# Kernel tuning notes

Hardware: AMD Instinct MI355X
Metric: run time of the kernel (lower is better)

Reference implementation:

```python
import jax, jax.numpy as jnp
import numpy as np

B, T, C = 1, 2048, 1024
H, HKV, DH, WIN = 16, 4, 64, 128
EPS = 1e-5


def rotate_half(x):
    x1, x2 = jnp.split(x, 2, axis=-1)
    return jnp.concatenate((-x2, x1), axis=-1)


def setup_inputs() -> dict:
    key = jax.random.key(0)
    ks = jax.random.split(key, 8)
    s = 0.02
    return {
        "x": jax.random.normal(ks[0], (B, T, C), dtype=jnp.float32),
        "Wq": jax.random.normal(ks[1], (C, H * DH), dtype=jnp.float32) * s,
        "Wk": jax.random.normal(ks[2], (C, HKV * DH), dtype=jnp.float32) * s,
        "Wv": jax.random.normal(ks[3], (C, HKV * DH), dtype=jnp.float32) * s,
        "Wc": jax.random.normal(ks[4], (C, C), dtype=jnp.float32) * s,
        "Wg": jax.random.normal(ks[5], (C, H), dtype=jnp.float32) * s,
        "bg": jax.random.normal(ks[6], (H,), dtype=jnp.float32) * s,
        "rms_w": jnp.ones((C,), dtype=jnp.float32),
    }


def reference(x, Wq, Wk, Wv, Wc, Wg, bg, rms_w):
    n_rep = H // HKV
    # projections -> [B, heads, T, DH]
    q = (x @ Wq).reshape(B, T, H, DH).transpose(0, 2, 1, 3)
    k = (x @ Wk).reshape(B, T, HKV, DH).transpose(0, 2, 1, 3)
    v = (x @ Wv).reshape(B, T, HKV, DH).transpose(0, 2, 1, 3)
    # rotary embedding (freqs duplicated across the two halves)
    inv_freq = 1.0 / (10000.0 ** (jnp.arange(0, DH, 2, dtype=jnp.float32) / DH))
    freqs = jnp.arange(T, dtype=jnp.float32)[:, None] * inv_freq[None, :]
    emb = jnp.concatenate((freqs, freqs), axis=-1)  # [T, DH]
    cos, sin = jnp.cos(emb)[None, None], jnp.sin(emb)[None, None]
    q = q * cos + rotate_half(q) * sin
    k = k * cos + rotate_half(k) * sin
    # GQA: repeat kv heads (contiguous repeat matches torch expand+reshape)
    k = jnp.repeat(k, n_rep, axis=1)
    v = jnp.repeat(v, n_rep, axis=1)
    # gated decay
    gate_logits = (x @ Wg + bg).reshape(B, T, H, 1).transpose(0, 2, 1, 3)  # [B,H,T,1]
    log_alpha = jax.nn.log_sigmoid(gate_logits)
    log_in_scale = jax.nn.log_sigmoid(-gate_logits)
    k_scaled = k * jnp.exp(log_in_scale)
    la_cum = jnp.cumsum(log_alpha, axis=2)                  # [B,H,T,1]
    log_decay = la_cum - jnp.swapaxes(la_cum, 2, 3)         # [B,H,T,T]
    causal = jnp.triu(jnp.ones((T, T), dtype=bool), k=1)
    decay = jnp.exp(jnp.where(causal, -jnp.inf, log_decay))
    scores = jnp.einsum('bhtd,bhsd->bhts', q, k_scaled)
    y_global = jnp.einsum('bhts,bhsd->bhtd', scores * decay, v)
    nb = T // WIN
    qb = q.reshape(B, H, nb, WIN, DH)
    kb = k.reshape(B, H, nb, WIN, DH)
    vb = v.reshape(B, H, nb, WIN, DH)
    att = jnp.einsum('bhnqd,bhnkd->bhnqk', qb, kb) / jnp.sqrt(jnp.float32(DH))
    wmask = jnp.triu(jnp.ones((WIN, WIN), dtype=bool), k=1)
    att = jax.nn.softmax(jnp.where(wmask, -jnp.inf, att), axis=-1)
    y_local = jnp.einsum('bhnqk,bhnkd->bhnqd', att, vb).reshape(B, H, T, DH)
    # fuse, RMSNorm, output projection
    y = (y_global + y_local).transpose(0, 2, 1, 3).reshape(B, T, C)
    y = y * jax.lax.rsqrt(jnp.mean(y * y, axis=-1, keepdims=True) + EPS) * rms_w
    return y @ Wc
```

## Files before the change

### kernel.cpp

```cpp
#include <hip/hip_runtime.h>
#include <hip/hip_bf16.h>


typedef __attribute__((ext_vector_type(8))) short bf16x8;
typedef __attribute__((ext_vector_type(4))) float f32x4;

#define MFMA16(a, b, c) __builtin_amdgcn_mfma_f32_16x16x32_bf16(a, b, c, 0, 0, 0)
#define LN10000_OVER_32 0.28782313662425575f

__device__ __forceinline__ short f2b(float f) {
  __hip_bfloat16 h = __float2bfloat16(f);
  return *reinterpret_cast<short*>(&h);
}
__device__ __forceinline__ float b2f(short s) {
  return __uint_as_float(((unsigned)(unsigned short)s) << 16);
}
__device__ __forceinline__ void gload16(const void* g, void* l) {
  __builtin_amdgcn_global_load_lds(
      (const __attribute__((address_space(1))) void*)g,
      (__attribute__((address_space(3))) void*)l, 16, 0, 0);
}

__device__ __forceinline__ void transpose_cvt_body(
    const float* __restrict__ src, short* __restrict__ dst, int R, int C,
    int bx, int by, float* ts ) {
  int c0 = bx * 32, r0 = by * 32;
  int tr = threadIdx.x >> 3, tc = (threadIdx.x & 7) * 4;
  float4 v = *(const float4*)&src[(size_t)(r0 + tr) * C + c0 + tc];
  ts[tr * 33 + tc] = v.x;
  ts[tr * 33 + tc + 1] = v.y;
  ts[tr * 33 + tc + 2] = v.z;
  ts[tr * 33 + tc + 3] = v.w;
  __syncthreads();
  alignas(8) short o[4];
#pragma unroll
  for (int i = 0; i < 4; ++i) o[i] = f2b(ts[(tc + i) * 33 + tr]);
  *(uint2*)&dst[(size_t)(c0 + tr) * R + r0 + tc] = *(uint2*)o;
}

__global__ __launch_bounds__(256) void prep_fused(
    const float* __restrict__ x, const float* __restrict__ Wq,
    const float* __restrict__ Wk, const float* __restrict__ Wv,
    const float* __restrict__ Wc, const float* __restrict__ Wg,
    const float* __restrict__ bg, short* __restrict__ xb,
    short* __restrict__ wqkvT, short* __restrict__ wcT,
    float* __restrict__ g) {
  __shared__ float ts[32 * 33];
  const int j = blockIdx.x;
  const int tid = threadIdx.x;
  if (j < 2048) {
    const int t = j;
    const int h = tid & 15, chunk = tid >> 4;
    const float* xr = x + (size_t)t * 1024 + chunk * 64;
    const float* wg = Wg + (size_t)chunk * 64 * 16 + h;
    float acc = 0.f;
#pragma unroll
    for (int c = 0; c < 64; c += 4) {
      float4 xv = *(const float4*)(xr + c);
      acc = fmaf(xv.x, wg[(c + 0) * 16], acc);
      acc = fmaf(xv.y, wg[(c + 1) * 16], acc);
      acc = fmaf(xv.z, wg[(c + 2) * 16], acc);
      acc = fmaf(xv.w, wg[(c + 3) * 16], acc);
    }
    ts[chunk * 16 + h] = acc;
    __syncthreads();
    if (tid < 16) {
      float s = bg[tid];
#pragma unroll
      for (int i = 0; i < 16; ++i) s += ts[i * 16 + tid];
      g[t * 16 + tid] = s;
    }
  } else if (j < 3072) {
    int i = ((j - 2048) * 256 + tid) * 8;
    float4 a = *(const float4*)(x + i);
    float4 b = *(const float4*)(x + i + 4);
    alignas(16) short o[8] = {f2b(a.x), f2b(a.y), f2b(a.z), f2b(a.w),
                              f2b(b.x), f2b(b.y), f2b(b.z), f2b(b.w)};
    *(float4*)(xb + i) = *(float4*)o;
  } else if (j < 4096) {
    int jj = j - 3072;
    transpose_cvt_body(Wq, wqkvT, 1024, 1024, jj & 31, jj >> 5, ts);
  } else if (j < 4352) {
    int jj = j - 4096;
    transpose_cvt_body(Wk, wqkvT + 1024 * 1024, 1024, 256, jj & 7, jj >> 3, ts);
  } else if (j < 4608) {
    int jj = j - 4352;
    transpose_cvt_body(Wv, wqkvT + 1280 * 1024, 1024, 256, jj & 7, jj >> 3, ts);
  } else {
    int jj = j - 4608;
    transpose_cvt_body(Wc, wcT, 1024, 1024, jj & 31, jj >> 5, ts);
  }
}

__global__ __launch_bounds__(256) void qkv_gemm_fused(
    const short* __restrict__ A, const short* __restrict__ Bt,
    short* __restrict__ qkvb, short* __restrict__ vtb,
    const float* __restrict__ g, float* __restrict__ lac,
    float* __restrict__ insc) {
  __shared__ short As[64 * 64];
  __shared__ short Bs[64 * 64];
  __shared__ float part[256];
  const int id = blockIdx.x;
  const int tid = threadIdx.x;
  if (id >= 768) {
    const int h = id - 768;
    float vals[8];
    float local = 0.f;
#pragma unroll
    for (int i = 0; i < 8; ++i) {
      int t = tid * 8 + i;
      float gv = g[t * 16 + h];
      float la = (gv > 0.f) ? -log1pf(expf(-gv)) : (gv - log1pf(expf(gv)));
      insc[h * 2048 + t] = 1.f / (1.f + expf(gv));
      vals[i] = la;
      local += la;
    }
    part[tid] = local;
    __syncthreads();
    for (int off = 1; off < 256; off <<= 1) {
      float add = (tid >= off) ? part[tid - off] : 0.f;
      __syncthreads();
      part[tid] += add;
      __syncthreads();
    }
    float run = (tid > 0) ? part[tid - 1] : 0.f;
#pragma unroll
    for (int i = 0; i < 8; ++i) {
      run += vals[i];
      lac[h * 2048 + tid * 8 + i] = run;
    }
    return;
  }
  const int lane = tid & 63, wid = tid >> 6;
  const int l15 = lane & 15, lq = lane >> 4;
  const int jlin = id >> 3;
  const int by = (id & 7) + 8 * (jlin / 24);
  const int bx = jlin % 24;
  const int m0 = by * 64, n0 = bx * 64;
  const int K = 1024;
  const int srow = lane >> 3;
  const int sc16 = (lane & 7) ^ srow;
  f32x4 acc[4];
#pragma unroll
  for (int nt = 0; nt < 4; ++nt) acc[nt] = {0.f, 0.f, 0.f, 0.f};
  for (int kt = 0; kt < K; kt += 64) {
    __syncthreads();
#pragma unroll
    for (int i = 0; i < 2; ++i) {
      int jj = wid * 2 + i;
      int row = jj * 8 + srow;
      gload16(A + (size_t)(m0 + row) * K + kt + sc16 * 8, &As[jj * 512]);
      gload16(Bt + (size_t)(n0 + row) * K + kt + sc16 * 8, &Bs[jj * 512]);
    }
    __syncthreads();
    bf16x8 af[2], bfr[4][2];
#pragma unroll
    for (int ks = 0; ks < 2; ++ks) {
      int c16 = ks * 4 + lq;
      int ar = wid * 16 + l15;
      af[ks] = *(const bf16x8*)&As[(ar * 8 + (c16 ^ (ar & 7))) * 8];
#pragma unroll
      for (int nt = 0; nt < 4; ++nt) {
        int br = nt * 16 + l15;
        bfr[nt][ks] = *(const bf16x8*)&Bs[(br * 8 + (c16 ^ (br & 7))) * 8];
      }
    }
#pragma unroll
    for (int ks = 0; ks < 2; ++ks)
#pragma unroll
      for (int nt = 0; nt < 4; ++nt)
        acc[nt] = MFMA16(af[ks], bfr[nt][ks], acc[nt]);
  }
  if (bx >= 20) {
    const int row0 = m0 + wid * 16 + lq * 4;
#pragma unroll
    for (int nt = 0; nt < 4; ++nt) {
      int vcol = (n0 - 1280) + nt * 16 + l15;
      alignas(8) short o4[4];
#pragma unroll
      for (int r = 0; r < 4; ++r) o4[r] = f2b(acc[nt][r]);
      *(uint2*)&vtb[(size_t)vcol * 2048 + row0] = *(uint2*)o4;
    }
    return;
  }
#pragma unroll
  for (int r = 0; r < 4; ++r) {
    int row_g = m0 + wid * 16 + lq * 4 + r;
    float t = (float)row_g;
#pragma unroll
    for (int nt = 0; nt < 2; ++nt) {
      int d = nt * 16 + l15;
      float th = t * __expf(-LN10000_OVER_32 * (float)d);
      float cs = cosf(th), sn = sinf(th);
      float a = acc[nt][r], b = acc[nt + 2][r];
      qkvb[(size_t)row_g * 1536 + n0 + d] = f2b(a * cs - b * sn);
      qkvb[(size_t)row_g * 1536 + n0 + d + 32] = f2b(b * cs + a * sn);
    }
  }
}

__global__ __launch_bounds__(256) void out_gemm(
    const short* __restrict__ A, const short* __restrict__ Bt,
    float* __restrict__ C, int M, int N, int K, int nbx) {
  __shared__ short As[64 * 64];
  __shared__ short Bs[64 * 64];
  const int tid = threadIdx.x, lane = tid & 63, wid = tid >> 6;
  const int l15 = lane & 15, lq = lane >> 4;
  const int id = blockIdx.x;
  const int jlin = id >> 3;
  const int by = (id & 7) + 8 * (jlin / nbx);
  const int bx = jlin % nbx;
  const int m0 = by * 64, n0 = bx * 64;
  const int srow = lane >> 3;
  const int sc16 = (lane & 7) ^ srow;
  f32x4 acc[4];
#pragma unroll
  for (int nt = 0; nt < 4; ++nt) acc[nt] = {0.f, 0.f, 0.f, 0.f};
  for (int kt = 0; kt < K; kt += 64) {
    __syncthreads();
#pragma unroll
    for (int i = 0; i < 2; ++i) {
      int jj = wid * 2 + i;
      int row = jj * 8 + srow;
      gload16(A + (size_t)(m0 + row) * K + kt + sc16 * 8, &As[jj * 512]);
      gload16(Bt + (size_t)(n0 + row) * K + kt + sc16 * 8, &Bs[jj * 512]);
    }
    __syncthreads();
    bf16x8 af[2], bfr[4][2];
#pragma unroll
    for (int ks = 0; ks < 2; ++ks) {
      int c16 = ks * 4 + lq;
      int ar = wid * 16 + l15;
      af[ks] = *(const bf16x8*)&As[(ar * 8 + (c16 ^ (ar & 7))) * 8];
#pragma unroll
      for (int nt = 0; nt < 4; ++nt) {
        int br = nt * 16 + l15;
        bfr[nt][ks] = *(const bf16x8*)&Bs[(br * 8 + (c16 ^ (br & 7))) * 8];
      }
    }
#pragma unroll
    for (int ks = 0; ks < 2; ++ks)
#pragma unroll
      for (int nt = 0; nt < 4; ++nt)
        acc[nt] = MFMA16(af[ks], bfr[nt][ks], acc[nt]);
  }
#pragma unroll
  for (int r = 0; r < 4; ++r) {
    int row_g = m0 + wid * 16 + lq * 4 + r;
#pragma unroll
    for (int nt = 0; nt < 4; ++nt)
      C[(size_t)row_g * N + n0 + nt * 16 + l15] = acc[nt][r];
  }
}

__global__ __launch_bounds__(256) void attn_fused(
    const short* __restrict__ qkv, const short* __restrict__ vtb,
    const float* __restrict__ lac, const float* __restrict__ insc,
    short* __restrict__ y0, short* __restrict__ y1, short* __restrict__ yl) {
  __shared__ short SA[64 * 64];
  __shared__ short SB[128 * 64];
  __shared__ short SC[64 * 128];
  __shared__ short SD[64 * 128];
  __shared__ float lacq[64], lacs[64], inss[64];
  const int tid = threadIdx.x, lane = tid & 63, wid = tid >> 6;
  const int l15 = lane & 15, lq = lane >> 4;
  const int h = blockIdx.y;
  const int kh = h >> 2;
  if (blockIdx.z == 0) {
    const int slot = blockIdx.x & 15, par = blockIdx.x >> 4;
    short* Qs = SA;
    short* Ks = SB;
    short* Vts = SC;
    short* Ps = SD;
    const int srow = lane >> 3;
    const int sc16 = (lane & 7) ^ srow;
    short* yout = par ? y1 : y0;
    for (int rep = 0; rep < 2; ++rep) {
      const int tt = rep ? 31 - slot : slot;
      __syncthreads();
#pragma unroll
      for (int i = 0; i < 2; ++i) {
        int jj = wid * 2 + i;
        int row = jj * 8 + srow;
        gload16(qkv + (size_t)(tt * 64 + row) * 1536 + h * 64 + sc16 * 8,
                &Qs[jj * 512]);
      }
      if (tid < 64) lacq[tid] = lac[h * 2048 + tt * 64 + tid];
      f32x4 o[4];
#pragma unroll
      for (int nt = 0; nt < 4; ++nt) o[nt] = {0.f, 0.f, 0.f, 0.f};
      for (int st = par; st <= tt; st += 2) {
        __syncthreads();
#pragma unroll
        for (int i = 0; i < 2; ++i) {
          int jj = wid * 2 + i;
          int row = jj * 8 + srow;
          gload16(qkv + (size_t)(st * 64 + row) * 1536 + 1024 + kh * 64 + sc16 * 8,
                  &Ks[jj * 512]);
          gload16(vtb + (size_t)(kh * 64 + row) * 2048 + st * 64 + sc16 * 8,
                  &Vts[jj * 512]);
        }
        if (tid < 64) {
          lacs[tid] = lac[h * 2048 + st * 64 + tid];
          inss[tid] = insc[h * 2048 + st * 64 + tid];
        }
        __syncthreads();
        const int qr = wid * 16 + l15;
        bf16x8 aq[2];
#pragma unroll
        for (int ks = 0; ks < 2; ++ks) {
          int c16 = ks * 4 + lq;
          aq[ks] = *(const bf16x8*)&Qs[(qr * 8 + (c16 ^ (qr & 7))) * 8];
        }
        f32x4 sv[4];
#pragma unroll
        for (int nt = 0; nt < 4; ++nt) {
          int kr = nt * 16 + l15;
          bf16x8 bk0 = *(const bf16x8*)&Ks[(kr * 8 + ((0 + lq) ^ (kr & 7))) * 8];
          bf16x8 bk1 = *(const bf16x8*)&Ks[(kr * 8 + ((4 + lq) ^ (kr & 7))) * 8];
          f32x4 z = {0.f, 0.f, 0.f, 0.f};
          z = MFMA16(aq[0], bk0, z);
          z = MFMA16(aq[1], bk1, z);
          sv[nt] = z;
        }
        const bool diag = (st == tt);
#pragma unroll
        for (int nt = 0; nt < 4; ++nt) {
          int col = nt * 16 + l15;
          float ls = lacs[col], is = inss[col];
#pragma unroll
          for (int r = 0; r < 4; ++r) {
            int row = wid * 16 + lq * 4 + r;
            float d = lacq[row] - ls;
            float w = __expf(fminf(d, 0.f)) * is;
            if (diag && col > row) w = 0.f;
            Ps[(row * 8 + ((col >> 3) ^ (row & 7))) * 8 + (col & 7)] =
                f2b(sv[nt][r] * w);
          }
        }
        __syncthreads();
        bf16x8 ap[2];
#pragma unroll
        for (int ks = 0; ks < 2; ++ks) {
          int c16 = ks * 4 + lq;
          ap[ks] = *(const bf16x8*)&Ps[(qr * 8 + (c16 ^ (qr & 7))) * 8];
        }
#pragma unroll
        for (int nt = 0; nt < 4; ++nt) {
          int vr = nt * 16 + l15;
          bf16x8 bv0 = *(const bf16x8*)&Vts[(vr * 8 + ((0 + lq) ^ (vr & 7))) * 8];
          bf16x8 bv1 = *(const bf16x8*)&Vts[(vr * 8 + ((4 + lq) ^ (vr & 7))) * 8];
          o[nt] = MFMA16(ap[0], bv0, o[nt]);
          o[nt] = MFMA16(ap[1], bv1, o[nt]);
        }
      }
#pragma unroll
      for (int nt = 0; nt < 4; ++nt)
#pragma unroll
        for (int r = 0; r < 4; ++r) {
          int row_g = tt * 64 + wid * 16 + lq * 4 + r;
          int colg = h * 64 + nt * 16 + l15;
          yout[(size_t)row_g * 1024 + colg] = f2b(o[nt][r]);
        }
    }
  } else {
    const int half = blockIdx.x & 1, wb = blockIdx.x >> 1;
    const int t0 = wb * 128;
    short* Qs = SA;
    short* Ks = SB;
    short* Vts = SC;
    short* Ps = SD;
#pragma unroll
    for (int i = 0; i < 2; ++i) {
      int c = tid + 256 * i;
      int row = c >> 3, cc = c & 7;
      *(float4*)&Qs[(row * 8 + (cc ^ (row & 7))) * 8] =
          *(const float4*)&qkv[(size_t)(t0 + half * 64 + row) * 1536 + h * 64 + cc * 8];
    }
#pragma unroll
    for (int i = 0; i < 4; ++i) {
      int c = tid + 256 * i;
      int row = c >> 3, cc = c & 7;
      *(float4*)&Ks[(row * 8 + (cc ^ (row & 7))) * 8] =
          *(const float4*)&qkv[(size_t)(t0 + row) * 1536 + 1024 + kh * 64 + cc * 8];
    }
#pragma unroll
    for (int i = 0; i < 4; ++i) {
      int c = tid + 256 * i;
      int row = c >> 4, cc = c & 15;
      int sw = (row * 16 + ((cc & 8) | ((cc & 7) ^ (row & 7)))) * 8;
      *(float4*)&Vts[sw] =
          *(const float4*)&vtb[(size_t)(kh * 64 + row) * 2048 + t0 + cc * 8];
    }
    __syncthreads();
    const int qr = wid * 16 + l15;
    bf16x8 aq[2];
#pragma unroll
    for (int ks = 0; ks < 2; ++ks) {
      int c16 = ks * 4 + lq;
      aq[ks] = *(const bf16x8*)&Qs[(qr * 8 + (c16 ^ (qr & 7))) * 8];
    }
    f32x4 sv[2][4];
    const int nst = half + 1;
    for (int st = 0; st < nst; ++st)
#pragma unroll
      for (int nt = 0; nt < 4; ++nt) {
        int kr = st * 64 + nt * 16 + l15;
        bf16x8 bk0 = *(const bf16x8*)&Ks[(kr * 8 + ((0 + lq) ^ (kr & 7))) * 8];
        bf16x8 bk1 = *(const bf16x8*)&Ks[(kr * 8 + ((4 + lq) ^ (kr & 7))) * 8];
        f32x4 z = {0.f, 0.f, 0.f, 0.f};
        z = MFMA16(aq[0], bk0, z);
        z = MFMA16(aq[1], bk1, z);
        sv[st][nt] = z;
      }
    float mrow[4], ssum[4];
#pragma unroll
    for (int r = 0; r < 4; ++r) mrow[r] = -1e30f;
    for (int st = 0; st < nst; ++st)
#pragma unroll
      for (int nt = 0; nt < 4; ++nt) {
        int col = st * 64 + nt * 16 + l15;
#pragma unroll
        for (int r = 0; r < 4; ++r) {
          int row = half * 64 + wid * 16 + lq * 4 + r;
          float v = (col <= row) ? sv[st][nt][r] * 0.125f : -1e30f;
          sv[st][nt][r] = v;
          mrow[r] = fmaxf(mrow[r], v);
        }
      }
#pragma unroll
    for (int r = 0; r < 4; ++r) {
      for (int off = 1; off < 16; off <<= 1)
        mrow[r] = fmaxf(mrow[r], __shfl_xor(mrow[r], off, 64));
      ssum[r] = 0.f;
    }
    for (int st = 0; st < nst; ++st)
#pragma unroll
      for (int nt = 0; nt < 4; ++nt) {
        int col = st * 64 + nt * 16 + l15;
#pragma unroll
        for (int r = 0; r < 4; ++r) {
          float e = __expf(sv[st][nt][r] - mrow[r]);
          ssum[r] += e;
          int row = wid * 16 + lq * 4 + r;
          int c16 = col >> 3;
          Ps[(row * 16 + ((c16 & 8) | ((c16 & 7) ^ (row & 7)))) * 8 + (col & 7)] =
              f2b(e);
        }
      }
#pragma unroll
    for (int r = 0; r < 4; ++r) {
      for (int off = 1; off < 16; off <<= 1) ssum[r] += __shfl_xor(ssum[r], off, 64);
      ssum[r] = 1.f / ssum[r];
    }
    __syncthreads();
    f32x4 o[4];
#pragma unroll
    for (int nt = 0; nt < 4; ++nt) o[nt] = {0.f, 0.f, 0.f, 0.f};
    for (int ks = 0; ks < nst * 2; ++ks) {
      int c16 = ks * 4 + lq;
      bf16x8 ap = *(const bf16x8*)&Ps[(qr * 16 + ((c16 & 8) | ((c16 & 7) ^ (qr & 7)))) * 8];
#pragma unroll
      for (int nt = 0; nt < 4; ++nt) {
        int vr = nt * 16 + l15;
        bf16x8 bv = *(const bf16x8*)&Vts[(vr * 16 + ((c16 & 8) | ((c16 & 7) ^ (vr & 7)))) * 8];
        o[nt] = MFMA16(ap, bv, o[nt]);
      }
    }
#pragma unroll
    for (int nt = 0; nt < 4; ++nt)
#pragma unroll
      for (int r = 0; r < 4; ++r) {
        int row_g = t0 + half * 64 + wid * 16 + lq * 4 + r;
        int colg = h * 64 + nt * 16 + l15;
        yl[(size_t)row_g * 1024 + colg] = f2b(o[nt][r] * ssum[r]);
      }
  }
}

__global__ __launch_bounds__(256) void rmsnorm_fuse(
    const short* __restrict__ y0, const short* __restrict__ y1,
    const short* __restrict__ ylc, const float* __restrict__ w,
    short* __restrict__ yn) {
  const int t = blockIdx.x, tid = threadIdx.x;
  __shared__ float red[4];
  __shared__ float rowv[1024];
  __shared__ float scale_sh;
  float ssum = 0.f;
  for (int c = tid; c < 1024; c += 256) {
    size_t idx = (size_t)t * 1024 + c;
    float v = b2f(y0[idx]) + b2f(y1[idx]) + b2f(ylc[idx]);
    rowv[c] = v;
    ssum = fmaf(v, v, ssum);
  }
  for (int off = 32; off > 0; off >>= 1) ssum += __shfl_down(ssum, off, 64);
  const int lane = tid & 63, wd = tid >> 6;
  if (lane == 0) red[wd] = ssum;
  __syncthreads();
  if (tid == 0)
    scale_sh = rsqrtf((red[0] + red[1] + red[2] + red[3]) * (1.0f / 1024.0f) + 1e-5f);
  __syncthreads();
  const float scale = scale_sh;
  for (int c = tid; c < 1024; c += 256)
    yn[(size_t)t * 1024 + c] = f2b(rowv[c] * scale * w[c]);
}

extern "C" void kernel_launch(void* const* d_in, const int* in_sizes, int n_in,
                              void* d_out, int out_size, void* d_ws,
                              size_t ws_size, hipStream_t stream) {
  const float* x = (const float*)d_in[0];
  const float* Wq = (const float*)d_in[1];
  const float* Wk = (const float*)d_in[2];
  const float* Wv = (const float*)d_in[3];
  const float* Wc = (const float*)d_in[4];
  const float* Wg = (const float*)d_in[5];
  const float* bg = (const float*)d_in[6];
  const float* rmsw = (const float*)d_in[7];
  float* out = (float*)d_out;

  short* wqkvT = (short*)d_ws;
  short* wcT = wqkvT + 1536 * 1024;
  short* qkvb = wcT + 1024 * 1024;
  short* vtb = qkvb + 2048 * 1536;
  float* gw = (float*)(vtb + 256 * 2048);
  float* lacw = gw + 2048 * 16;
  float* inscw = lacw + 16 * 2048;
  short* xb = (short*)(inscw + 16 * 2048);
  short* y0 = xb;
  short* y1 = xb + 2048 * 1024;
  short* ylc = y1 + 2048 * 1024;
  short* yn = ylc + 2048 * 1024;

  prep_fused<<<5632, 256, 0, stream>>>(x, Wq, Wk, Wv, Wc, Wg, bg, xb, wqkvT,
                                       wcT, gw);
  qkv_gemm_fused<<<784, 256, 0, stream>>>(xb, wqkvT, qkvb, vtb, gw, lacw,
                                          inscw);
  attn_fused<<<dim3(32, 16, 2), 256, 0, stream>>>(qkvb, vtb, lacw, inscw, y0,
                                                  y1, ylc);
  rmsnorm_fuse<<<2048, 256, 0, stream>>>(y0, y1, ylc, rmsw, yn);
  out_gemm<<<512, 256, 0, stream>>>(yn, wcT, out, 2048, 1024, 1024, 16);
}
```

Before: 150.3 us.

## Replace quadratic gated-decay attention with chunked linear-attention state scan

Computes the global gated-decay attention as a chunked recurrence. Per-chunk K^T V state contributions are built with MFMA, a sequential scan over chunks forms prefix states in bf16, and each chunk combines intra-chunk masked attention with Q times the carried state. The QKV GEMM also writes a transposed K copy for the state products, and the rmsnorm now sums two inputs instead of three. This removes the O(T^2) tile loop, at the cost of extra launches, a serial scan with low parallelism, and bf16 rounding of the carried state.

```diff
diff --git a/kernel.cpp b/kernel.cpp
--- a/kernel.cpp
+++ b/kernel.cpp
@@ -95,8 +95,8 @@
 __global__ __launch_bounds__(256) void qkv_gemm_fused(
     const short* __restrict__ A, const short* __restrict__ Bt,
     short* __restrict__ qkvb, short* __restrict__ vtb,
-    const float* __restrict__ g, float* __restrict__ lac,
-    float* __restrict__ insc) {
+    short* __restrict__ ktb, const float* __restrict__ g,
+    float* __restrict__ lac, float* __restrict__ insc) {
   __shared__ short As[64 * 64];
   __shared__ short Bs[64 * 64];
   __shared__ float part[256];
@@ -171,8 +171,8 @@
       for (int nt = 0; nt < 4; ++nt)
         acc[nt] = MFMA16(af[ks], bfr[nt][ks], acc[nt]);
   }
+  const int row0 = m0 + wid * 16 + lq * 4;
   if (bx >= 20) {
-    const int row0 = m0 + wid * 16 + lq * 4;
 #pragma unroll
     for (int nt = 0; nt < 4; ++nt) {
       int vcol = (n0 - 1280) + nt * 16 + l15;
@@ -183,20 +183,385 @@
     }
     return;
   }
-#pragma unroll
-  for (int r = 0; r < 4; ++r) {
-    int row_g = m0 + wid * 16 + lq * 4 + r;
-    float t = (float)row_g;
-#pragma unroll
-    for (int nt = 0; nt < 2; ++nt) {
-      int d = nt * 16 + l15;
-      float th = t * __expf(-LN10000_OVER_32 * (float)d);
+  const bool isk = (bx >= 16);
+#pragma unroll
+  for (int nt = 0; nt < 2; ++nt) {
+    int d = nt * 16 + l15;
+    float ivf = __expf(-LN10000_OVER_32 * (float)d);
+    alignas(8) short oa[4], ob[4];
+#pragma unroll
+    for (int r = 0; r < 4; ++r) {
+      int row_g = row0 + r;
+      float th = (float)row_g * ivf;
       float cs = cosf(th), sn = sinf(th);
       float a = acc[nt][r], b = acc[nt + 2][r];
-      qkvb[(size_t)row_g * 1536 + n0 + d] = f2b(a * cs - b * sn);
-      qkvb[(size_t)row_g * 1536 + n0 + d + 32] = f2b(b * cs + a * sn);
-    }
-  }
+      oa[r] = f2b(a * cs - b * sn);
+      ob[r] = f2b(b * cs + a * sn);
+      qkvb[(size_t)row_g * 1536 + n0 + d] = oa[r];
+      qkvb[(size_t)row_g * 1536 + n0 + d + 32] = ob[r];
+    }
+    if (isk) {
+      int dk = n0 - 1024 + d;
+      *(uint2*)&ktb[(size_t)dk * 2048 + row0] = *(uint2*)oa;
+      *(uint2*)&ktb[(size_t)(dk + 32) * 2048 + row0] = *(uint2*)ob;
+    }
+  }
+}
+
+__global__ __launch_bounds__(256) void p1_local(
+    const short* __restrict__ qkv, const short* __restrict__ vtb,
+    const short* __restrict__ ktb, const float* __restrict__ lac,
+    const float* __restrict__ insc, float* __restrict__ Bmat,
+    short* __restrict__ yl) {
+  __shared__ short SA[64 * 64];
+  __shared__ short SB[128 * 64];
+  __shared__ short SC[64 * 128];
+  __shared__ short SD[64 * 128];
+  __shared__ float lacs[64], inss[64], gvals[64];
+  const int tid = threadIdx.x, lane = tid & 63, wid = tid >> 6;
+  const int l15 = lane & 15, lq = lane >> 4;
+  const int h = blockIdx.y;
+  const int kh = h >> 2;
+  if (blockIdx.z == 0) {
+    const int c = blockIdx.x;
+    short* Ks = SB;
+    short* Vts = SC;
+    const int srow = lane >> 3;
+    const int sc16 = (lane & 7) ^ srow;
+#pragma unroll
+    for (int i = 0; i < 2; ++i) {
+      int jj = wid * 2 + i;
+      int row = jj * 8 + srow;
+      gload16(ktb + (size_t)(kh * 64 + row) * 2048 + c * 64 + sc16 * 8,
+              &Ks[jj * 512]);
+      gload16(vtb + (size_t)(kh * 64 + row) * 2048 + c * 64 + sc16 * 8,
+              &Vts[jj * 512]);
+    }
+    if (tid < 64) {
+      lacs[tid] = lac[h * 2048 + c * 64 + tid];
+      inss[tid] = insc[h * 2048 + c * 64 + tid];
+    }
+    __syncthreads();
+    if (tid < 64)
+      gvals[tid] = __expf(fminf(lacs[63] - lacs[tid], 0.f)) * inss[tid];
+    __syncthreads();
+    const int er = wid * 16 + l15;
+    bf16x8 av[2];
+#pragma unroll
+    for (int ks = 0; ks < 2; ++ks) {
+      int c16 = ks * 4 + lq;
+      bf16x8 raw = *(const bf16x8*)&Vts[(er * 8 + (c16 ^ (er & 7))) * 8];
+      float4 g0 = *(const float4*)&gvals[c16 * 8];
+      float4 g1 = *(const float4*)&gvals[c16 * 8 + 4];
+      float gv[8] = {g0.x, g0.y, g0.z, g0.w, g1.x, g1.y, g1.z, g1.w};
+      bf16x8 sc;
+#pragma unroll
+      for (int jx = 0; jx < 8; ++jx) sc[jx] = f2b(b2f(raw[jx]) * gv[jx]);
+      av[ks] = sc;
+    }
+    f32x4 acc[4];
+#pragma unroll
+    for (int nt = 0; nt < 4; ++nt) acc[nt] = {0.f, 0.f, 0.f, 0.f};
+#pragma unroll
+    for (int ks = 0; ks < 2; ++ks) {
+      int c16 = ks * 4 + lq;
+#pragma unroll
+      for (int nt = 0; nt < 4; ++nt) {
+        int dr = nt * 16 + l15;
+        bf16x8 bk = *(const bf16x8*)&Ks[(dr * 8 + (c16 ^ (dr & 7))) * 8];
+        acc[nt] = MFMA16(av[ks], bk, acc[nt]);
+      }
+    }
+    float* Bout = Bmat + (size_t)(h * 32 + c) * 4096;
+#pragma unroll
+    for (int nt = 0; nt < 4; ++nt)
+#pragma unroll
+      for (int r = 0; r < 4; ++r) {
+        int e = wid * 16 + lq * 4 + r;
+        Bout[e * 64 + nt * 16 + l15] = acc[nt][r];
+      }
+  } else {
+    const int half = blockIdx.x & 1, wb = blockIdx.x >> 1;
+    const int t0 = wb * 128;
+    short* Qs = SA;
+    short* Ks = SB;
+    short* Vts = SC;
+    short* Ps = SD;
+#pragma unroll
+    for (int i = 0; i < 2; ++i) {
+      int cix = tid + 256 * i;
+      int row = cix >> 3, cc = cix & 7;
+      *(float4*)&Qs[(row * 8 + (cc ^ (row & 7))) * 8] =
+          *(const float4*)&qkv[(size_t)(t0 + half * 64 + row) * 1536 + h * 64 + cc * 8];
+    }
+#pragma unroll
+    for (int i = 0; i < 4; ++i) {
+      int cix = tid + 256 * i;
+      int row = cix >> 3, cc = cix & 7;
+      *(float4*)&Ks[(row * 8 + (cc ^ (row & 7))) * 8] =
+          *(const float4*)&qkv[(size_t)(t0 + row) * 1536 + 1024 + kh * 64 + cc * 8];
+    }
+#pragma unroll
+    for (int i = 0; i < 4; ++i) {
+      int cix = tid + 256 * i;
+      int row = cix >> 4, cc = cix & 15;
+      int sw = (row * 16 + ((cc & 8) | ((cc & 7) ^ (row & 7)))) * 8;
+      *(float4*)&Vts[sw] =
+          *(const float4*)&vtb[(size_t)(kh * 64 + row) * 2048 + t0 + cc * 8];
+    }
+    __syncthreads();
+    const int qr = wid * 16 + l15;
+    bf16x8 aq[2];
+#pragma unroll
+    for (int ks = 0; ks < 2; ++ks) {
+      int c16 = ks * 4 + lq;
+      aq[ks] = *(const bf16x8*)&Qs[(qr * 8 + (c16 ^ (qr & 7))) * 8];
+    }
+    f32x4 sv[2][4];
+    const int nst = half + 1;
+    for (int st = 0; st < nst; ++st)
+#pragma unroll
+      for (int nt = 0; nt < 4; ++nt) {
+        int kr = st * 64 + nt * 16 + l15;
+        bf16x8 bk0 = *(const bf16x8*)&Ks[(kr * 8 + ((0 + lq) ^ (kr & 7))) * 8];
+        bf16x8 bk1 = *(const bf16x8*)&Ks[(kr * 8 + ((4 + lq) ^ (kr & 7))) * 8];
+        f32x4 z = {0.f, 0.f, 0.f, 0.f};
+        z = MFMA16(aq[0], bk0, z);
+        z = MFMA16(aq[1], bk1, z);
+        sv[st][nt] = z;
+      }
+    float mrow[4], ssum[4];
+#pragma unroll
+    for (int r = 0; r < 4; ++r) mrow[r] = -1e30f;
+    for (int st = 0; st < nst; ++st)
+#pragma unroll
+      for (int nt = 0; nt < 4; ++nt) {
+        int col = st * 64 + nt * 16 + l15;
+#pragma unroll
+        for (int r = 0; r < 4; ++r) {
+          int row = half * 64 + wid * 16 + lq * 4 + r;
+          float v = (col <= row) ? sv[st][nt][r] * 0.125f : -1e30f;
+          sv[st][nt][r] = v;
+          mrow[r] = fmaxf(mrow[r], v);
+        }
+      }
+#pragma unroll
+    for (int r = 0; r < 4; ++r) {
+      for (int off = 1; off < 16; off <<= 1)
+        mrow[r] = fmaxf(mrow[r], __shfl_xor(mrow[r], off, 64));
+      ssum[r] = 0.f;
+    }
+    for (int st = 0; st < nst; ++st)
+#pragma unroll
+      for (int nt = 0; nt < 4; ++nt) {
+        int col = st * 64 + nt * 16 + l15;
+#pragma unroll
+        for (int r = 0; r < 4; ++r) {
+          float e = __expf(sv[st][nt][r] - mrow[r]);
+          ssum[r] += e;
+          int row = wid * 16 + lq * 4 + r;
+          int c16 = col >> 3;
+          Ps[(row * 16 + ((c16 & 8) | ((c16 & 7) ^ (row & 7)))) * 8 + (col & 7)] =
+              f2b(e);
+        }
+      }
+#pragma unroll
+    for (int r = 0; r < 4; ++r) {
+      for (int off = 1; off < 16; off <<= 1) ssum[r] += __shfl_xor(ssum[r], off, 64);
+      ssum[r] = 1.f / ssum[r];
+    }
+    __syncthreads();
+    f32x4 o[4];
+#pragma unroll
+    for (int nt = 0; nt < 4; ++nt) o[nt] = {0.f, 0.f, 0.f, 0.f};
+    for (int ks = 0; ks < nst * 2; ++ks) {
+      int c16 = ks * 4 + lq;
+      bf16x8 ap = *(const bf16x8*)&Ps[(qr * 16 + ((c16 & 8) | ((c16 & 7) ^ (qr & 7)))) * 8];
+#pragma unroll
+      for (int nt = 0; nt < 4; ++nt) {
+        int vr = nt * 16 + l15;
+        bf16x8 bv = *(const bf16x8*)&Vts[(vr * 16 + ((c16 & 8) | ((c16 & 7) ^ (vr & 7)))) * 8];
+        o[nt] = MFMA16(ap, bv, o[nt]);
+      }
+    }
+#pragma unroll
+    for (int nt = 0; nt < 4; ++nt)
+#pragma unroll
+      for (int r = 0; r < 4; ++r) {
+        int row_g = t0 + half * 64 + wid * 16 + lq * 4 + r;
+        int colg = h * 64 + nt * 16 + l15;
+        yl[(size_t)row_g * 1024 + colg] = f2b(o[nt][r] * ssum[r]);
+      }
+  }
+}
+
+__global__ __launch_bounds__(256) void scan_kernel(
+    const float* __restrict__ Bmat, const float* __restrict__ lac,
+    short* __restrict__ St) {
+  const int h = blockIdx.x, tid = threadIdx.x;
+  __shared__ float lacE[32];
+  if (tid < 32) lacE[tid] = lac[h * 2048 + tid * 64 + 63];
+  __syncthreads();
+  const int base = tid * 16;
+  float S[16];
+#pragma unroll
+  for (int i = 0; i < 16; ++i) S[i] = 0.f;
+  alignas(16) short z16[16];
+#pragma unroll
+  for (int i = 0; i < 16; ++i) z16[i] = 0;
+  *(uint4*)&St[(size_t)(h * 32) * 4096 + base] = *(uint4*)z16;
+  *(uint4*)&St[(size_t)(h * 32) * 4096 + base + 8] = *(uint4*)(z16 + 8);
+  for (int c = 1; c < 32; ++c) {
+    float a = (c >= 2) ? __expf(fminf(lacE[c - 1] - lacE[c - 2], 0.f)) : 0.f;
+    const float* Bp = Bmat + (size_t)(h * 32 + c - 1) * 4096 + base;
+    float4 b0 = *(const float4*)(Bp + 0);
+    float4 b1 = *(const float4*)(Bp + 4);
+    float4 b2 = *(const float4*)(Bp + 8);
+    float4 b3 = *(const float4*)(Bp + 12);
+    float bb[16] = {b0.x, b0.y, b0.z, b0.w, b1.x, b1.y, b1.z, b1.w,
+                    b2.x, b2.y, b2.z, b2.w, b3.x, b3.y, b3.z, b3.w};
+    alignas(16) short o16[16];
+#pragma unroll
+    for (int i = 0; i < 16; ++i) {
+      S[i] = fmaf(a, S[i], bb[i]);
+      o16[i] = f2b(S[i]);
+    }
+    *(uint4*)&St[(size_t)(h * 32 + c) * 4096 + base] = *(uint4*)o16;
+    *(uint4*)&St[(size_t)(h * 32 + c) * 4096 + base + 8] = *(uint4*)(o16 + 8);
+  }
+}
+
+__global__ __launch_bounds__(256) void global_attn_v3(
+    const short* __restrict__ qkv, const short* __restrict__ vtb,
+    const short* __restrict__ St, const float* __restrict__ lac,
+    const float* __restrict__ insc, short* __restrict__ yg) {
+  const int c = blockIdx.x, h = blockIdx.y;
+  const int kh = h >> 2;
+  __shared__ short Qs[64 * 64], Ks[64 * 64], Vts[64 * 64], Sts[64 * 64],
+      Ps[64 * 64];
+  __shared__ float lacq[64], inss[64];
+  __shared__ float laprev_sh;
+  const int tid = threadIdx.x, lane = tid & 63, wid = tid >> 6;
+  const int l15 = lane & 15, lq = lane >> 4;
+  const int srow = lane >> 3;
+  const int sc16 = (lane & 7) ^ srow;
+#pragma unroll
+  for (int i = 0; i < 2; ++i) {
+    int jj = wid * 2 + i;
+    int row = jj * 8 + srow;
+    gload16(qkv + (size_t)(c * 64 + row) * 1536 + h * 64 + sc16 * 8,
+            &Qs[jj * 512]);
+    gload16(qkv + (size_t)(c * 64 + row) * 1536 + 1024 + kh * 64 + sc16 * 8,
+            &Ks[jj * 512]);
+    gload16(vtb + (size_t)(kh * 64 + row) * 2048 + c * 64 + sc16 * 8,
+            &Vts[jj * 512]);
+    gload16(St + (size_t)(h * 32 + c) * 4096 + row * 64 + sc16 * 8,
+            &Sts[jj * 512]);
+  }
+  if (tid < 64) {
+    lacq[tid] = lac[h * 2048 + c * 64 + tid];
+    inss[tid] = insc[h * 2048 + c * 64 + tid];
+  }
+  if (tid == 0) laprev_sh = (c > 0) ? lac[h * 2048 + c * 64 - 1] : 1e30f;
+  __syncthreads();
+  const int qr = wid * 16 + l15;
+  bf16x8 aq[2];
+#pragma unroll
+  for (int ks = 0; ks < 2; ++ks) {
+    int c16 = ks * 4 + lq;
+    aq[ks] = *(const bf16x8*)&Qs[(qr * 8 + (c16 ^ (qr & 7))) * 8];
+  }
+  f32x4 sv[4];
+#pragma unroll
+  for (int nt = 0; nt < 4; ++nt) {
+    int kr = nt * 16 + l15;
+    bf16x8 bk0 = *(const bf16x8*)&Ks[(kr * 8 + ((0 + lq) ^ (kr & 7))) * 8];
+    bf16x8 bk1 = *(const bf16x8*)&Ks[(kr * 8 + ((4 + lq) ^ (kr & 7))) * 8];
+    f32x4 z = {0.f, 0.f, 0.f, 0.f};
+    z = MFMA16(aq[0], bk0, z);
+    z = MFMA16(aq[1], bk1, z);
+    sv[nt] = z;
+  }
+#pragma unroll
+  for (int nt = 0; nt < 4; ++nt) {
+    int col = nt * 16 + l15;
+    float ls = lacq[col], is = inss[col];
+#pragma unroll
+    for (int r = 0; r < 4; ++r) {
+      int row = wid * 16 + lq * 4 + r;
+      float d = lacq[row] - ls;
+      float w = __expf(fminf(d, 0.f)) * is;
+      if (col > row) w = 0.f;
+      Ps[(row * 8 + ((col >> 3) ^ (row & 7))) * 8 + (col & 7)] = f2b(sv[nt][r] * w);
+    }
+  }
+  f32x4 oi[4];
+#pragma unroll
+  for (int nt = 0; nt < 4; ++nt) {
+    int er = nt * 16 + l15;
+    bf16x8 bs0 = *(const bf16x8*)&Sts[(er * 8 + ((0 + lq) ^ (er & 7))) * 8];
+    bf16x8 bs1 = *(const bf16x8*)&Sts[(er * 8 + ((4 + lq) ^ (er & 7))) * 8];
+    f32x4 z = {0.f, 0.f, 0.f, 0.f};
+    z = MFMA16(aq[0], bs0, z);
+    z = MFMA16(aq[1], bs1, z);
+    oi[nt] = z;
+  }
+  __syncthreads();
+  bf16x8 ap[2];
+#pragma unroll
+  for (int ks = 0; ks < 2; ++ks) {
+    int c16 = ks * 4 + lq;
+    ap[ks] = *(const bf16x8*)&Ps[(qr * 8 + (c16 ^ (qr & 7))) * 8];
+  }
+  f32x4 o[4];
+#pragma unroll
+  for (int nt = 0; nt < 4; ++nt) {
+    int vr = nt * 16 + l15;
+    bf16x8 bv0 = *(const bf16x8*)&Vts[(vr * 8 + ((0 + lq) ^ (vr & 7))) * 8];
+    bf16x8 bv1 = *(const bf16x8*)&Vts[(vr * 8 + ((4 + lq) ^ (vr & 7))) * 8];
+    f32x4 z = {0.f, 0.f, 0.f, 0.f};
+    z = MFMA16(ap[0], bv0, z);
+    z = MFMA16(ap[1], bv1, z);
+    o[nt] = z;
+  }
+  const float laprev = laprev_sh;
+#pragma unroll
+  for (int r = 0; r < 4; ++r) {
+    int row = wid * 16 + lq * 4 + r;
+    float rfac = __expf(fminf(lacq[row] - laprev, 0.f));
+    int row_g = c * 64 + row;
+#pragma unroll
+    for (int nt = 0; nt < 4; ++nt) {
+      int colg = h * 64 + nt * 16 + l15;
+      yg[(size_t)row_g * 1024 + colg] = f2b(o[nt][r] + rfac * oi[nt][r]);
+    }
+  }
+}
+
+__global__ __launch_bounds__(256) void rmsnorm_fuse(
+    const short* __restrict__ yg, const short* __restrict__ ylc,
+    const float* __restrict__ w, short* __restrict__ yn) {
+  const int t = blockIdx.x, tid = threadIdx.x;
+  __shared__ float red[4];
+  __shared__ float rowv[1024];
+  __shared__ float scale_sh;
+  float ssum = 0.f;
+  for (int c = tid; c < 1024; c += 256) {
+    size_t idx = (size_t)t * 1024 + c;
+    float v = b2f(yg[idx]) + b2f(ylc[idx]);
+    rowv[c] = v;
+    ssum = fmaf(v, v, ssum);
+  }
+  for (int off = 32; off > 0; off >>= 1) ssum += __shfl_down(ssum, off, 64);
+  const int lane = tid & 63, wd = tid >> 6;
+  if (lane == 0) red[wd] = ssum;
+  __syncthreads();
+  if (tid == 0)
+    scale_sh = rsqrtf((red[0] + red[1] + red[2] + red[3]) * (1.0f / 1024.0f) + 1e-5f);
+  __syncthreads();
+  const float scale = scale_sh;
+  for (int c = tid; c < 1024; c += 256)
+    yn[(size_t)t * 1024 + c] = f2b(rowv[c] * scale * w[c]);
 }
 
 __global__ __launch_bounds__(256) void out_gemm(
@@ -253,258 +618,6 @@
   }
 }
 
-__global__ __launch_bounds__(256) void attn_fused(
-    const short* __restrict__ qkv, const short* __restrict__ vtb,
-    const float* __restrict__ lac, const float* __restrict__ insc,
-    short* __restrict__ y0, short* __restrict__ y1, short* __restrict__ yl) {
-  __shared__ short SA[64 * 64];
-  __shared__ short SB[128 * 64];
-  __shared__ short SC[64 * 128];
-  __shared__ short SD[64 * 128];
-  __shared__ float lacq[64], lacs[64], inss[64];
-  const int tid = threadIdx.x, lane = tid & 63, wid = tid >> 6;
-  const int l15 = lane & 15, lq = lane >> 4;
-  const int h = blockIdx.y;
-  const int kh = h >> 2;
-  if (blockIdx.z == 0) {
-    const int slot = blockIdx.x & 15, par = blockIdx.x >> 4;
-    short* Qs = SA;
-    short* Ks = SB;
-    short* Vts = SC;
-    short* Ps = SD;
-    const int srow = lane >> 3;
-    const int sc16 = (lane & 7) ^ srow;
-    short* yout = par ? y1 : y0;
-    for (int rep = 0; rep < 2; ++rep) {
-      const int tt = rep ? 31 - slot : slot;
-      __syncthreads();
-#pragma unroll
-      for (int i = 0; i < 2; ++i) {
-        int jj = wid * 2 + i;
-        int row = jj * 8 + srow;
-        gload16(qkv + (size_t)(tt * 64 + row) * 1536 + h * 64 + sc16 * 8,
-                &Qs[jj * 512]);
-      }
-      if (tid < 64) lacq[tid] = lac[h * 2048 + tt * 64 + tid];
-      f32x4 o[4];
-#pragma unroll
-      for (int nt = 0; nt < 4; ++nt) o[nt] = {0.f, 0.f, 0.f, 0.f};
-      for (int st = par; st <= tt; st += 2) {
-        __syncthreads();
-#pragma unroll
-        for (int i = 0; i < 2; ++i) {
-          int jj = wid * 2 + i;
-          int row = jj * 8 + srow;
-          gload16(qkv + (size_t)(st * 64 + row) * 1536 + 1024 + kh * 64 + sc16 * 8,
-                  &Ks[jj * 512]);
-          gload16(vtb + (size_t)(kh * 64 + row) * 2048 + st * 64 + sc16 * 8,
-                  &Vts[jj * 512]);
-        }
-        if (tid < 64) {
-          lacs[tid] = lac[h * 2048 + st * 64 + tid];
-          inss[tid] = insc[h * 2048 + st * 64 + tid];
-        }
-        __syncthreads();
-        const int qr = wid * 16 + l15;
-        bf16x8 aq[2];
-#pragma unroll
-        for (int ks = 0; ks < 2; ++ks) {
-          int c16 = ks * 4 + lq;
-          aq[ks] = *(const bf16x8*)&Qs[(qr * 8 + (c16 ^ (qr & 7))) * 8];
-        }
-        f32x4 sv[4];
-#pragma unroll
-        for (int nt = 0; nt < 4; ++nt) {
-          int kr = nt * 16 + l15;
-          bf16x8 bk0 = *(const bf16x8*)&Ks[(kr * 8 + ((0 + lq) ^ (kr & 7))) * 8];
-          bf16x8 bk1 = *(const bf16x8*)&Ks[(kr * 8 + ((4 + lq) ^ (kr & 7))) * 8];
-          f32x4 z = {0.f, 0.f, 0.f, 0.f};
-          z = MFMA16(aq[0], bk0, z);
-          z = MFMA16(aq[1], bk1, z);
-          sv[nt] = z;
-        }
-        const bool diag = (st == tt);
-#pragma unroll
-        for (int nt = 0; nt < 4; ++nt) {
-          int col = nt * 16 + l15;
-          float ls = lacs[col], is = inss[col];
-#pragma unroll
-          for (int r = 0; r < 4; ++r) {
-            int row = wid * 16 + lq * 4 + r;
-            float d = lacq[row] - ls;
-            float w = __expf(fminf(d, 0.f)) * is;
-            if (diag && col > row) w = 0.f;
-            Ps[(row * 8 + ((col >> 3) ^ (row & 7))) * 8 + (col & 7)] =
-                f2b(sv[nt][r] * w);
-          }
-        }
-        __syncthreads();
-        bf16x8 ap[2];
-#pragma unroll
-        for (int ks = 0; ks < 2; ++ks) {
-          int c16 = ks * 4 + lq;
-          ap[ks] = *(const bf16x8*)&Ps[(qr * 8 + (c16 ^ (qr & 7))) * 8];
-        }
-#pragma unroll
-        for (int nt = 0; nt < 4; ++nt) {
-          int vr = nt * 16 + l15;
-          bf16x8 bv0 = *(const bf16x8*)&Vts[(vr * 8 + ((0 + lq) ^ (vr & 7))) * 8];
-          bf16x8 bv1 = *(const bf16x8*)&Vts[(vr * 8 + ((4 + lq) ^ (vr & 7))) * 8];
-          o[nt] = MFMA16(ap[0], bv0, o[nt]);
-          o[nt] = MFMA16(ap[1], bv1, o[nt]);
-        }
-      }
-#pragma unroll
-      for (int nt = 0; nt < 4; ++nt)
-#pragma unroll
-        for (int r = 0; r < 4; ++r) {
-          int row_g = tt * 64 + wid * 16 + lq * 4 + r;
-          int colg = h * 64 + nt * 16 + l15;
-          yout[(size_t)row_g * 1024 + colg] = f2b(o[nt][r]);
-        }
-    }
-  } else {
-    const int half = blockIdx.x & 1, wb = blockIdx.x >> 1;
-    const int t0 = wb * 128;
-    short* Qs = SA;
-    short* Ks = SB;
-    short* Vts = SC;
-    short* Ps = SD;
-#pragma unroll
-    for (int i = 0; i < 2; ++i) {
-      int c = tid + 256 * i;
-      int row = c >> 3, cc = c & 7;
-      *(float4*)&Qs[(row * 8 + (cc ^ (row & 7))) * 8] =
-          *(const float4*)&qkv[(size_t)(t0 + half * 64 + row) * 1536 + h * 64 + cc * 8];
-    }
-#pragma unroll
-    for (int i = 0; i < 4; ++i) {
-      int c = tid + 256 * i;
-      int row = c >> 3, cc = c & 7;
-      *(float4*)&Ks[(row * 8 + (cc ^ (row & 7))) * 8] =
-          *(const float4*)&qkv[(size_t)(t0 + row) * 1536 + 1024 + kh * 64 + cc * 8];
-    }
-#pragma unroll
-    for (int i = 0; i < 4; ++i) {
-      int c = tid + 256 * i;
-      int row = c >> 4, cc = c & 15;
-      int sw = (row * 16 + ((cc & 8) | ((cc & 7) ^ (row & 7)))) * 8;
-      *(float4*)&Vts[sw] =
-          *(const float4*)&vtb[(size_t)(kh * 64 + row) * 2048 + t0 + cc * 8];
-    }
-    __syncthreads();
-    const int qr = wid * 16 + l15;
-    bf16x8 aq[2];
-#pragma unroll
-    for (int ks = 0; ks < 2; ++ks) {
-      int c16 = ks * 4 + lq;
-      aq[ks] = *(const bf16x8*)&Qs[(qr * 8 + (c16 ^ (qr & 7))) * 8];
-    }
-    f32x4 sv[2][4];
-    const int nst = half + 1;
-    for (int st = 0; st < nst; ++st)
-#pragma unroll
-      for (int nt = 0; nt < 4; ++nt) {
-        int kr = st * 64 + nt * 16 + l15;
-        bf16x8 bk0 = *(const bf16x8*)&Ks[(kr * 8 + ((0 + lq) ^ (kr & 7))) * 8];
-        bf16x8 bk1 = *(const bf16x8*)&Ks[(kr * 8 + ((4 + lq) ^ (kr & 7))) * 8];
-        f32x4 z = {0.f, 0.f, 0.f, 0.f};
-        z = MFMA16(aq[0], bk0, z);
-        z = MFMA16(aq[1], bk1, z);
-        sv[st][nt] = z;
-      }
-    float mrow[4], ssum[4];
-#pragma unroll
-    for (int r = 0; r < 4; ++r) mrow[r] = -1e30f;
-    for (int st = 0; st < nst; ++st)
-#pragma unroll
-      for (int nt = 0; nt < 4; ++nt) {
-        int col = st * 64 + nt * 16 + l15;
-#pragma unroll
-        for (int r = 0; r < 4; ++r) {
-          int row = half * 64 + wid * 16 + lq * 4 + r;
-          float v = (col <= row) ? sv[st][nt][r] * 0.125f : -1e30f;
-          sv[st][nt][r] = v;
-          mrow[r] = fmaxf(mrow[r], v);
-        }
-      }
-#pragma unroll
-    for (int r = 0; r < 4; ++r) {
-      for (int off = 1; off < 16; off <<= 1)
-        mrow[r] = fmaxf(mrow[r], __shfl_xor(mrow[r], off, 64));
-      ssum[r] = 0.f;
-    }
-    for (int st = 0; st < nst; ++st)
-#pragma unroll
-      for (int nt = 0; nt < 4; ++nt) {
-        int col = st * 64 + nt * 16 + l15;
-#pragma unroll
-        for (int r = 0; r < 4; ++r) {
-          float e = __expf(sv[st][nt][r] - mrow[r]);
-          ssum[r] += e;
-          int row = wid * 16 + lq * 4 + r;
-          int c16 = col >> 3;
-          Ps[(row * 16 + ((c16 & 8) | ((c16 & 7) ^ (row & 7)))) * 8 + (col & 7)] =
-              f2b(e);
-        }
-      }
-#pragma unroll
-    for (int r = 0; r < 4; ++r) {
-      for (int off = 1; off < 16; off <<= 1) ssum[r] += __shfl_xor(ssum[r], off, 64);
-      ssum[r] = 1.f / ssum[r];
-    }
-    __syncthreads();
-    f32x4 o[4];
-#pragma unroll
-    for (int nt = 0; nt < 4; ++nt) o[nt] = {0.f, 0.f, 0.f, 0.f};
-    for (int ks = 0; ks < nst * 2; ++ks) {
-      int c16 = ks * 4 + lq;
-      bf16x8 ap = *(const bf16x8*)&Ps[(qr * 16 + ((c16 & 8) | ((c16 & 7) ^ (qr & 7)))) * 8];
-#pragma unroll
-      for (int nt = 0; nt < 4; ++nt) {
-        int vr = nt * 16 + l15;
-        bf16x8 bv = *(const bf16x8*)&Vts[(vr * 16 + ((c16 & 8) | ((c16 & 7) ^ (vr & 7)))) * 8];
-        o[nt] = MFMA16(ap, bv, o[nt]);
-      }
-    }
-#pragma unroll
-    for (int nt = 0; nt < 4; ++nt)
-#pragma unroll
-      for (int r = 0; r < 4; ++r) {
-        int row_g = t0 + half * 64 + wid * 16 + lq * 4 + r;
-        int colg = h * 64 + nt * 16 + l15;
-        yl[(size_t)row_g * 1024 + colg] = f2b(o[nt][r] * ssum[r]);
-      }
-  }
-}
-
-__global__ __launch_bounds__(256) void rmsnorm_fuse(
-    const short* __restrict__ y0, const short* __restrict__ y1,
-    const short* __restrict__ ylc, const float* __restrict__ w,
-    short* __restrict__ yn) {
-  const int t = blockIdx.x, tid = threadIdx.x;
-  __shared__ float red[4];
-  __shared__ float rowv[1024];
-  __shared__ float scale_sh;
-  float ssum = 0.f;
-  for (int c = tid; c < 1024; c += 256) {
-    size_t idx = (size_t)t * 1024 + c;
-    float v = b2f(y0[idx]) + b2f(y1[idx]) + b2f(ylc[idx]);
-    rowv[c] = v;
-    ssum = fmaf(v, v, ssum);
-  }
-  for (int off = 32; off > 0; off >>= 1) ssum += __shfl_down(ssum, off, 64);
-  const int lane = tid & 63, wd = tid >> 6;
-  if (lane == 0) red[wd] = ssum;
-  __syncthreads();
-  if (tid == 0)
-    scale_sh = rsqrtf((red[0] + red[1] + red[2] + red[3]) * (1.0f / 1024.0f) + 1e-5f);
-  __syncthreads();
-  const float scale = scale_sh;
-  for (int c = tid; c < 1024; c += 256)
-    yn[(size_t)t * 1024 + c] = f2b(rowv[c] * scale * w[c]);
-}
-
 extern "C" void kernel_launch(void* const* d_in, const int* in_sizes, int n_in,
                               void* d_out, int out_size, void* d_ws,
                               size_t ws_size, hipStream_t stream) {
@@ -522,21 +635,26 @@
   short* wcT = wqkvT + 1536 * 1024;
   short* qkvb = wcT + 1024 * 1024;
   short* vtb = qkvb + 2048 * 1536;
-  float* gw = (float*)(vtb + 256 * 2048);
+  short* ktb = vtb + 256 * 2048;
+  float* gw = (float*)(ktb + 256 * 2048);
   float* lacw = gw + 2048 * 16;
   float* inscw = lacw + 16 * 2048;
-  short* xb = (short*)(inscw + 16 * 2048);
-  short* y0 = xb;
-  short* y1 = xb + 2048 * 1024;
-  short* ylc = y1 + 2048 * 1024;
+  float* Bmat = inscw + 16 * 2048;
+  short* Stb = (short*)(Bmat + 16 * 32 * 4096);
+  short* xb = Stb + 16 * 32 * 4096;
+  short* yg = xb;
+  short* ylc = xb + 2048 * 1024;
   short* yn = ylc + 2048 * 1024;
 
   prep_fused<<<5632, 256, 0, stream>>>(x, Wq, Wk, Wv, Wc, Wg, bg, xb, wqkvT,
                                        wcT, gw);
-  qkv_gemm_fused<<<784, 256, 0, stream>>>(xb, wqkvT, qkvb, vtb, gw, lacw,
+  qkv_gemm_fused<<<784, 256, 0, stream>>>(xb, wqkvT, qkvb, vtb, ktb, gw, lacw,
                                           inscw);
-  attn_fused<<<dim3(32, 16, 2), 256, 0, stream>>>(qkvb, vtb, lacw, inscw, y0,
-                                                  y1, ylc);
-  rmsnorm_fuse<<<2048, 256, 0, stream>>>(y0, y1, ylc, rmsw, yn);
+  p1_local<<<dim3(32, 16, 2), 256, 0, stream>>>(qkvb, vtb, ktb, lacw, inscw,
+                                                Bmat, ylc);
+  scan_kernel<<<16, 256, 0, stream>>>(Bmat, lacw, Stb);
+  global_attn_v3<<<dim3(32, 16), 256, 0, stream>>>(qkvb, vtb, Stb, lacw, inscw,
+                                                   yg);
+  rmsnorm_fuse<<<2048, 256, 0, stream>>>(yg, ylc, rmsw, yn);
   out_gemm<<<512, 256, 0, stream>>>(yn, wcT, out, 2048, 1024, 1024, 16);
 }
```

Result: faster. 147.1 us (-2.1%).
